# Performance work log

Hardware: AMD Instinct MI355X
Metric: run time of the kernel (lower is better)

Reference implementation:

```python
import jax, jax.numpy as jnp
import numpy as np

N_NODES = 50000


def binarize(w):
    # straight-through sign binarization (forward: sign, backward: identity)
    return w + jax.lax.stop_gradient(jnp.sign(w) - w)


def sage_conv(x, src, dst, w_l, b_l, w_r, num_nodes):
    # PyG SAGEConv with mean aggregation:
    # out[i] = lin_l(mean_{j in N(i)} x[j]) + lin_r(x[i])
    msgs = x[src]  # [E, F] gather from source nodes
    agg = jax.ops.segment_sum(msgs, dst, num_segments=num_nodes)  # [N, F]
    deg = jax.ops.segment_sum(jnp.ones_like(dst, dtype=x.dtype), dst,
                              num_segments=num_nodes)
    agg = agg / jnp.maximum(deg, 1.0)[:, None]
    return agg @ w_l.T + b_l + x @ w_r.T


def setup_inputs() -> dict:
    key = jax.random.key(0)
    ks = jax.random.split(key, 9)
    in_dim, hid, out_dim = 96, 128, 64
    x = jax.random.normal(ks[0], (N_NODES, in_dim), dtype=jnp.float32)
    edge_index = jax.random.randint(ks[1], (2, 800000), 0, N_NODES, dtype=jnp.int64)
    s1 = 1.0 / np.sqrt(in_dim)
    s2 = 1.0 / np.sqrt(hid)
    w1_l = jax.random.uniform(ks[2], (hid, in_dim), minval=-s1, maxval=s1)
    b1 = jax.random.uniform(ks[3], (hid,), minval=-s1, maxval=s1)
    w1_r = jax.random.uniform(ks[4], (hid, in_dim), minval=-s1, maxval=s1)
    w2_l = jax.random.uniform(ks[5], (out_dim, hid), minval=-s2, maxval=s2)
    b2 = jax.random.uniform(ks[6], (out_dim,), minval=-s2, maxval=s2)
    w2_r = jax.random.uniform(ks[7], (out_dim, hid), minval=-s2, maxval=s2)
    return {"x": x, "edge_index": edge_index, "w1_l": w1_l, "b1": b1,
            "w1_r": w1_r, "w2_l": w2_l, "b2": b2, "w2_r": w2_r}


def reference(x, edge_index, w1_l, b1, w1_r, w2_l, b2, w2_r):
    src, dst = edge_index[0], edge_index[1]
    h = sage_conv(x, src, dst, binarize(w1_l), b1, binarize(w1_r), N_NODES)
    h = jax.nn.relu(h)
    out = sage_conv(h, src, dst, binarize(w2_l), b2, binarize(w2_r), N_NODES)
    return jnp.squeeze(out, axis=-1) if out.shape[-1] == 1 else out
```

## Files before the change

### kernel.cpp

```cpp
#include <hip/hip_runtime.h>
#include <cstdint>
#include <cstddef>


#define N_NODES 50000
#define IN_DIM 96
#define HID 128
#define OUT_DIM 64
#define DCAP 64

typedef __attribute__((ext_vector_type(8))) short bf16x8;
typedef __attribute__((ext_vector_type(4))) float f32x4;

static inline size_t alignUp(size_t v, size_t a) { return (v + a - 1) & ~(a - 1); }

__device__ __forceinline__ uint16_t f2bf(float f) {
  uint32_t u = __float_as_uint(f);
  return (uint16_t)((u + 0x7FFF + ((u >> 16) & 1)) >> 16);
}
__device__ __forceinline__ float bflo(uint32_t v) { return __uint_as_float(v << 16); }
__device__ __forceinline__ float bfhi(uint32_t v) { return __uint_as_float(v & 0xFFFF0000u); }

__device__ __forceinline__ uint16_t sgnbf(float w) {
  return (w > 0.f) ? (uint16_t)0x3F80 : ((w < 0.f) ? (uint16_t)0xBF80 : (uint16_t)0);
}

#define NS1 (128 * 192)
#define NS2 (128 * 128)
#define NSCAT 1024

__global__ __launch_bounds__(256) void build_prep_kernel(
    const int* __restrict__ src, const int* __restrict__ dst,
    int* __restrict__ cnt, uint16_t* __restrict__ adj16, int E,
    const float* __restrict__ x,
    const float* __restrict__ w1l, const float* __restrict__ w1r,
    const float* __restrict__ w2l, const float* __restrict__ w2r,
    uint16_t* __restrict__ S1t, uint16_t* __restrict__ S2t,
    uint16_t* __restrict__ xb, int total4) {
  const int t = threadIdx.x;
  if ((int)blockIdx.x < NSCAT) {
    const int stride = NSCAT * 256;
    for (int i = blockIdx.x * 256 + t; i < E; i += stride) {
      const int d = dst[i];
      const int s = src[i];
      const int k = atomicAdd(&cnt[d], 1);
      if (k < DCAP) adj16[(d << 6) + k] = (uint16_t)s;
    }
  } else {
    const int idx = ((int)blockIdx.x - NSCAT) * 256 + t;
    if (idx < NS1) {
      int n = idx / 192, k = idx - n * 192;
      float w = (k < 96) ? w1l[n * 96 + k] : w1r[n * 96 + (k - 96)];
      S1t[idx] = sgnbf(w);
    } else if (idx < NS1 + NS2) {
      int i2 = idx - NS1;
      int n = i2 >> 7, k = i2 & 127;
      float w = (n < 64) ? w2l[n * 128 + k] : w2r[(n - 64) * 128 + k];
      S2t[i2] = sgnbf(w);
    } else {
      int i = idx - NS1 - NS2;
      if (i < total4) {
        float4 v = *(const float4*)(x + (size_t)i * 4);
        uint32_t p0 = (uint32_t)f2bf(v.x) | ((uint32_t)f2bf(v.y) << 16);
        uint32_t p1 = (uint32_t)f2bf(v.z) | ((uint32_t)f2bf(v.w) << 16);
        *(uint2*)(xb + (size_t)i * 4) = make_uint2(p0, p1);
      }
    }
  }
}

__global__ __launch_bounds__(256) void agg1_kernel(const uint16_t* __restrict__ xb,
    const uint16_t* __restrict__ adj16, const int* __restrict__ cnt,
    uint16_t* __restrict__ AGGb, int nNodes) {
  const int sg = threadIdx.x >> 4;
  const int j = threadIdx.x & 15;
  const int n = blockIdx.x * 16 + sg;
  if (n >= nNodes) return;
  const int deg = min(cnt[n], DCAP);
  const int beg = n << 6;
  const int end = beg + deg;
  const bool act = j < 12;
  const int foff = j * 8;
  float a0 = 0.f, a1 = 0.f, a2 = 0.f, a3 = 0.f, a4 = 0.f, a5 = 0.f, a6 = 0.f, a7 = 0.f;

  int e = beg;
  for (; e + 8 <= end; e += 8) {
    const uint4 av = *(const uint4*)(adj16 + e);
    const uint32_t s0 = av.x & 0xFFFFu, s1 = av.x >> 16;
    const uint32_t s2 = av.y & 0xFFFFu, s3 = av.y >> 16;
    const uint32_t s4 = av.z & 0xFFFFu, s5 = av.z >> 16;
    const uint32_t s6 = av.w & 0xFFFFu, s7 = av.w >> 16;
    uint4 v0 = make_uint4(0u,0u,0u,0u), v1 = v0, v2 = v0, v3 = v0;
    uint4 v4 = v0, v5 = v0, v6 = v0, v7 = v0;
    if (act) {
      v0 = *(const uint4*)(xb + (size_t)s0 * IN_DIM + foff);
      v1 = *(const uint4*)(xb + (size_t)s1 * IN_DIM + foff);
      v2 = *(const uint4*)(xb + (size_t)s2 * IN_DIM + foff);
      v3 = *(const uint4*)(xb + (size_t)s3 * IN_DIM + foff);
      v4 = *(const uint4*)(xb + (size_t)s4 * IN_DIM + foff);
      v5 = *(const uint4*)(xb + (size_t)s5 * IN_DIM + foff);
      v6 = *(const uint4*)(xb + (size_t)s6 * IN_DIM + foff);
      v7 = *(const uint4*)(xb + (size_t)s7 * IN_DIM + foff);
    }
    __builtin_amdgcn_sched_barrier(0);
    a0 += (bflo(v0.x) + bflo(v1.x) + bflo(v2.x) + bflo(v3.x)) + (bflo(v4.x) + bflo(v5.x) + bflo(v6.x) + bflo(v7.x));
    a1 += (bfhi(v0.x) + bfhi(v1.x) + bfhi(v2.x) + bfhi(v3.x)) + (bfhi(v4.x) + bfhi(v5.x) + bfhi(v6.x) + bfhi(v7.x));
    a2 += (bflo(v0.y) + bflo(v1.y) + bflo(v2.y) + bflo(v3.y)) + (bflo(v4.y) + bflo(v5.y) + bflo(v6.y) + bflo(v7.y));
    a3 += (bfhi(v0.y) + bfhi(v1.y) + bfhi(v2.y) + bfhi(v3.y)) + (bfhi(v4.y) + bfhi(v5.y) + bfhi(v6.y) + bfhi(v7.y));
    a4 += (bflo(v0.z) + bflo(v1.z) + bflo(v2.z) + bflo(v3.z)) + (bflo(v4.z) + bflo(v5.z) + bflo(v6.z) + bflo(v7.z));
    a5 += (bfhi(v0.z) + bfhi(v1.z) + bfhi(v2.z) + bfhi(v3.z)) + (bfhi(v4.z) + bfhi(v5.z) + bfhi(v6.z) + bfhi(v7.z));
    a6 += (bflo(v0.w) + bflo(v1.w) + bflo(v2.w) + bflo(v3.w)) + (bflo(v4.w) + bflo(v5.w) + bflo(v6.w) + bflo(v7.w));
    a7 += (bfhi(v0.w) + bfhi(v1.w) + bfhi(v2.w) + bfhi(v3.w)) + (bfhi(v4.w) + bfhi(v5.w) + bfhi(v6.w) + bfhi(v7.w));
  }
  if (e + 4 <= end) {
    const uint2 av = *(const uint2*)(adj16 + e);
    const uint32_t s0 = av.x & 0xFFFFu, s1 = av.x >> 16;
    const uint32_t s2 = av.y & 0xFFFFu, s3 = av.y >> 16;
    uint4 v0 = make_uint4(0u,0u,0u,0u), v1 = v0, v2 = v0, v3 = v0;
    if (act) {
      v0 = *(const uint4*)(xb + (size_t)s0 * IN_DIM + foff);
      v1 = *(const uint4*)(xb + (size_t)s1 * IN_DIM + foff);
      v2 = *(const uint4*)(xb + (size_t)s2 * IN_DIM + foff);
      v3 = *(const uint4*)(xb + (size_t)s3 * IN_DIM + foff);
    }
    __builtin_amdgcn_sched_barrier(0);
    a0 += bflo(v0.x) + bflo(v1.x) + bflo(v2.x) + bflo(v3.x);
    a1 += bfhi(v0.x) + bfhi(v1.x) + bfhi(v2.x) + bfhi(v3.x);
    a2 += bflo(v0.y) + bflo(v1.y) + bflo(v2.y) + bflo(v3.y);
    a3 += bfhi(v0.y) + bfhi(v1.y) + bfhi(v2.y) + bfhi(v3.y);
    a4 += bflo(v0.z) + bflo(v1.z) + bflo(v2.z) + bflo(v3.z);
    a5 += bfhi(v0.z) + bfhi(v1.z) + bfhi(v2.z) + bfhi(v3.z);
    a6 += bflo(v0.w) + bflo(v1.w) + bflo(v2.w) + bflo(v3.w);
    a7 += bfhi(v0.w) + bfhi(v1.w) + bfhi(v2.w) + bfhi(v3.w);
    e += 4;
  }
  for (; e < end; ++e) {
    const uint32_t s = adj16[e];
    uint4 v = make_uint4(0u,0u,0u,0u);
    if (act) v = *(const uint4*)(xb + (size_t)s * IN_DIM + foff);
    a0 += bflo(v.x); a1 += bfhi(v.x);
    a2 += bflo(v.y); a3 += bfhi(v.y);
    a4 += bflo(v.z); a5 += bfhi(v.z);
    a6 += bflo(v.w); a7 += bfhi(v.w);
  }
  if (act) {
    const float inv = 1.0f / (float)(deg > 1 ? deg : 1);
    uint4 o;
    o.x = (uint32_t)f2bf(a0 * inv) | ((uint32_t)f2bf(a1 * inv) << 16);
    o.y = (uint32_t)f2bf(a2 * inv) | ((uint32_t)f2bf(a3 * inv) << 16);
    o.z = (uint32_t)f2bf(a4 * inv) | ((uint32_t)f2bf(a5 * inv) << 16);
    o.w = (uint32_t)f2bf(a6 * inv) | ((uint32_t)f2bf(a7 * inv) << 16);
    *(uint4*)(AGGb + (size_t)n * IN_DIM + foff) = o;
  }
}

__global__ __launch_bounds__(256) void final_kernel(const uint16_t* __restrict__ T2b,
    const float* __restrict__ R2, const uint16_t* __restrict__ adj16,
    const int* __restrict__ cnt, float* __restrict__ out, int nNodes) {
  const int sg = threadIdx.x >> 4;
  const int j = threadIdx.x & 15;
  const int n = blockIdx.x * 16 + sg;
  if (n >= nNodes) return;
  const int deg = min(cnt[n], DCAP);
  const int beg = n << 6;
  const int end = beg + deg;
  const int foff = j * 4;
  float a0 = 0.f, a1 = 0.f, a2 = 0.f, a3 = 0.f;

  int e = beg;
  for (; e + 8 <= end; e += 8) {
    const uint4 av = *(const uint4*)(adj16 + e);
    const uint32_t s0 = av.x & 0xFFFFu, s1 = av.x >> 16;
    const uint32_t s2 = av.y & 0xFFFFu, s3 = av.y >> 16;
    const uint32_t s4 = av.z & 0xFFFFu, s5 = av.z >> 16;
    const uint32_t s6 = av.w & 0xFFFFu, s7 = av.w >> 16;
    const uint2 v0 = *(const uint2*)(T2b + (size_t)s0 * 64 + foff);
    const uint2 v1 = *(const uint2*)(T2b + (size_t)s1 * 64 + foff);
    const uint2 v2 = *(const uint2*)(T2b + (size_t)s2 * 64 + foff);
    const uint2 v3 = *(const uint2*)(T2b + (size_t)s3 * 64 + foff);
    const uint2 v4 = *(const uint2*)(T2b + (size_t)s4 * 64 + foff);
    const uint2 v5 = *(const uint2*)(T2b + (size_t)s5 * 64 + foff);
    const uint2 v6 = *(const uint2*)(T2b + (size_t)s6 * 64 + foff);
    const uint2 v7 = *(const uint2*)(T2b + (size_t)s7 * 64 + foff);
    __builtin_amdgcn_sched_barrier(0);
    a0 += (bflo(v0.x) + bflo(v1.x) + bflo(v2.x) + bflo(v3.x)) + (bflo(v4.x) + bflo(v5.x) + bflo(v6.x) + bflo(v7.x));
    a1 += (bfhi(v0.x) + bfhi(v1.x) + bfhi(v2.x) + bfhi(v3.x)) + (bfhi(v4.x) + bfhi(v5.x) + bfhi(v6.x) + bfhi(v7.x));
    a2 += (bflo(v0.y) + bflo(v1.y) + bflo(v2.y) + bflo(v3.y)) + (bflo(v4.y) + bflo(v5.y) + bflo(v6.y) + bflo(v7.y));
    a3 += (bfhi(v0.y) + bfhi(v1.y) + bfhi(v2.y) + bfhi(v3.y)) + (bfhi(v4.y) + bfhi(v5.y) + bfhi(v6.y) + bfhi(v7.y));
  }
  if (e + 4 <= end) {
    const uint2 av = *(const uint2*)(adj16 + e);
    const uint32_t s0 = av.x & 0xFFFFu, s1 = av.x >> 16;
    const uint32_t s2 = av.y & 0xFFFFu, s3 = av.y >> 16;
    const uint2 v0 = *(const uint2*)(T2b + (size_t)s0 * 64 + foff);
    const uint2 v1 = *(const uint2*)(T2b + (size_t)s1 * 64 + foff);
    const uint2 v2 = *(const uint2*)(T2b + (size_t)s2 * 64 + foff);
    const uint2 v3 = *(const uint2*)(T2b + (size_t)s3 * 64 + foff);
    __builtin_amdgcn_sched_barrier(0);
    a0 += bflo(v0.x) + bflo(v1.x) + bflo(v2.x) + bflo(v3.x);
    a1 += bfhi(v0.x) + bfhi(v1.x) + bfhi(v2.x) + bfhi(v3.x);
    a2 += bflo(v0.y) + bflo(v1.y) + bflo(v2.y) + bflo(v3.y);
    a3 += bfhi(v0.y) + bfhi(v1.y) + bfhi(v2.y) + bfhi(v3.y);
    e += 4;
  }
  for (; e < end; ++e) {
    const uint32_t s = adj16[e];
    const uint2 v = *(const uint2*)(T2b + (size_t)s * 64 + foff);
    a0 += bflo(v.x); a1 += bfhi(v.x);
    a2 += bflo(v.y); a3 += bfhi(v.y);
  }
  const float inv = 1.0f / (float)(deg > 1 ? deg : 1);
  const float4 r = *(const float4*)(R2 + (size_t)n * 64 + foff);
  float4 o;
  o.x = a0 * inv + r.x;
  o.y = a1 * inv + r.y;
  o.z = a2 * inv + r.z;
  o.w = a3 * inv + r.w;
  *(float4*)(out + (size_t)n * 64 + foff) = o;
}

#define SP1 200
#define SP2 136
#define HP 136
__global__ __launch_bounds__(256) void gemm12_kernel(
    const uint16_t* __restrict__ AGGb, const uint16_t* __restrict__ xb,
    const uint16_t* __restrict__ S1t, const uint16_t* __restrict__ S2t,
    const float* __restrict__ b1, const float* __restrict__ b2,
    uint16_t* __restrict__ T2b, float* __restrict__ R2, int M) {
  __shared__ uint16_t BS[128 * SP1];
  __shared__ uint16_t Hs[64 * HP];
  const int tid = threadIdx.x;
  const int wv = tid >> 6;
  const int lane = tid & 63;
  const int m16 = lane & 15;
  const int quad = lane >> 4;
  const int rowBase = blockIdx.x * 64 + wv * 16;
  int arow = rowBase + m16;
  if (arow >= M) arow = M - 1;
  const int kq = quad * 8;

#pragma unroll
  for (int i = 0; i < 12; ++i) {
    const int idx8 = tid + i * 256;
    const int col = idx8 / 24;
    const int k8 = (idx8 - col * 24) * 8;
    const bf16x8 v = *(const bf16x8*)(S1t + (size_t)idx8 * 8);
    *(bf16x8*)&BS[col * SP1 + k8] = v;
  }
  bf16x8 a1f[6];
#pragma unroll
  for (int s = 0; s < 3; ++s)
    a1f[s] = *(const bf16x8*)(AGGb + (size_t)arow * IN_DIM + s * 32 + kq);
#pragma unroll
  for (int s = 0; s < 3; ++s)
    a1f[3 + s] = *(const bf16x8*)(xb + (size_t)arow * IN_DIM + s * 32 + kq);
  __syncthreads();

  f32x4 acc1[8];
#pragma unroll
  for (int cf = 0; cf < 8; ++cf) acc1[cf] = (f32x4){0.f, 0.f, 0.f, 0.f};
#pragma unroll
  for (int s = 0; s < 6; ++s) {
#pragma unroll
    for (int cf = 0; cf < 8; ++cf) {
      const bf16x8 b = *(const bf16x8*)&BS[(cf * 16 + m16) * SP1 + s * 32 + kq];
      acc1[cf] = __builtin_amdgcn_mfma_f32_16x16x32_bf16(a1f[s], b, acc1[cf], 0, 0, 0);
    }
  }

#pragma unroll
  for (int cf = 0; cf < 8; ++cf) {
    const int col = cf * 16 + m16;
    const float bias = b1[col];
#pragma unroll
    for (int r = 0; r < 4; ++r) {
      const float v = fmaxf(acc1[cf][r] + bias, 0.f);
      Hs[(wv * 16 + quad * 4 + r) * HP + col] = f2bf(v);
    }
  }
  __syncthreads();

#pragma unroll
  for (int i = 0; i < 8; ++i) {
    const int idx8 = tid + i * 256;
    const int col = idx8 >> 4;
    const int k8 = (idx8 & 15) * 8;
    const bf16x8 v = *(const bf16x8*)(S2t + (size_t)idx8 * 8);
    *(bf16x8*)&BS[col * SP2 + k8] = v;
  }
  __syncthreads();

  f32x4 acc2[8];
#pragma unroll
  for (int cf = 0; cf < 8; ++cf) acc2[cf] = (f32x4){0.f, 0.f, 0.f, 0.f};
#pragma unroll
  for (int s = 0; s < 4; ++s) {
    const bf16x8 a = *(const bf16x8*)&Hs[(wv * 16 + m16) * HP + s * 32 + kq];
#pragma unroll
    for (int cf = 0; cf < 8; ++cf) {
      const bf16x8 b = *(const bf16x8*)&BS[(cf * 16 + m16) * SP2 + s * 32 + kq];
      acc2[cf] = __builtin_amdgcn_mfma_f32_16x16x32_bf16(a, b, acc2[cf], 0, 0, 0);
    }
  }

#pragma unroll
  for (int cf = 0; cf < 8; ++cf) {
    const int col = cf * 16 + m16;
#pragma unroll
    for (int r = 0; r < 4; ++r) {
      const int row = rowBase + quad * 4 + r;
      if (row < M) {
        const float v = acc2[cf][r];
        if (col < 64) {
          T2b[(size_t)row * 64 + col] = f2bf(v);
        } else {
          R2[(size_t)row * 64 + (col - 64)] = v + b2[col - 64];
        }
      }
    }
  }
}

extern "C" void kernel_launch(void* const* d_in, const int* in_sizes, int n_in,
                              void* d_out, int out_size, void* d_ws, size_t ws_size,
                              hipStream_t stream) {
  const float* x   = (const float*)d_in[0];
  const int*   ei  = (const int*)d_in[1];
  const float* w1l = (const float*)d_in[2];
  const float* b1  = (const float*)d_in[3];
  const float* w1r = (const float*)d_in[4];
  const float* w2l = (const float*)d_in[5];
  const float* b2  = (const float*)d_in[6];
  const float* w2r = (const float*)d_in[7];
  float* out = (float*)d_out;

  const int N = in_sizes[0] / IN_DIM;
  const int E = in_sizes[1] / 2;
  const int* src = ei;
  const int* dst = ei + E;

  char* p = (char*)d_ws;
  uint16_t* AGGb = (uint16_t*)p; p += alignUp((size_t)N * IN_DIM * sizeof(uint16_t), 256);
  uint16_t* T2b  = (uint16_t*)p; p += alignUp((size_t)N * 64 * sizeof(uint16_t), 256);
  float* R2      = (float*)p;    p += alignUp((size_t)N * 64 * sizeof(float), 256);
  uint16_t* xb = (uint16_t*)p; p += alignUp((size_t)N * IN_DIM * sizeof(uint16_t), 256);
  uint16_t* S1t = (uint16_t*)p; p += alignUp(NS1 * sizeof(uint16_t), 256);
  uint16_t* S2t = (uint16_t*)p; p += alignUp(NS2 * sizeof(uint16_t), 256);
  uint16_t* adj16 = (uint16_t*)p; p += alignUp((size_t)N * DCAP * sizeof(uint16_t), 256);
  int* cnt = (int*)p; p += alignUp((size_t)N * sizeof(int), 256);
  (void)ws_size; (void)n_in; (void)out_size;

  hipMemsetAsync(cnt, 0, (size_t)N * sizeof(int), stream);

  const int total4 = N * IN_DIM / 4;
  const int prepThreads = NS1 + NS2 + total4;
  const int nPrep = (prepThreads + 255) / 256;
  build_prep_kernel<<<NSCAT + nPrep, 256, 0, stream>>>(
      src, dst, cnt, adj16, E,
      x, w1l, w1r, w2l, w2r, S1t, S2t, xb, total4);

  const int nodeBlocks16 = (N + 15) / 16;
  agg1_kernel<<<nodeBlocks16, 256, 0, stream>>>(xb, adj16, cnt, AGGb, N);

  const int gemmBlocks = (N + 63) / 64;
  gemm12_kernel<<<gemmBlocks, 256, 0, stream>>>(AGGb, xb, S1t, S2t, b1, b2, T2b, R2, N);

  final_kernel<<<nodeBlocks16, 256, 0, stream>>>(T2b, R2, adj16, cnt, out, N);
}
```

Measured before the change: 190.8 us.

## Build adjacency via two-pass bucketed scatter with shared-memory atomics

Replaces the per-edge global atomicAdd on node counters with a two-pass approach. First, edges are binned into 256-node buckets using shared-memory histograms and one global atomic per bucket per chunk. Then a per-bucket kernel builds node counts and adjacency lists with shared-memory atomics. This targets global atomic contention and scattered writes, at the cost of an extra kernel, a large staging buffer, and a fixed bucket capacity (CAP) that could overflow and drop edges.

```diff
diff --git a/kernel.cpp b/kernel.cpp
--- a/kernel.cpp
+++ b/kernel.cpp
@@ -8,6 +8,7 @@
 #define HID 128
 #define OUT_DIM 64
 #define DCAP 64
+#define CAP 6144
 
 typedef __attribute__((ext_vector_type(8))) short bf16x8;
 typedef __attribute__((ext_vector_type(4))) float f32x4;
@@ -27,27 +28,40 @@
 
 #define NS1 (128 * 192)
 #define NS2 (128 * 128)
-#define NSCAT 1024
-
-__global__ __launch_bounds__(256) void build_prep_kernel(
+#define SCAT_CHUNK 2048
+
+__global__ __launch_bounds__(256) void scatter_prep_kernel(
     const int* __restrict__ src, const int* __restrict__ dst,
-    int* __restrict__ cnt, uint16_t* __restrict__ adj16, int E,
+    int* __restrict__ bucketCursor, uint32_t* __restrict__ bucketBuf,
+    int E, int nScat,
     const float* __restrict__ x,
     const float* __restrict__ w1l, const float* __restrict__ w1r,
     const float* __restrict__ w2l, const float* __restrict__ w2r,
     uint16_t* __restrict__ S1t, uint16_t* __restrict__ S2t,
     uint16_t* __restrict__ xb, int total4) {
+  __shared__ int h[256];
+  __shared__ int g[256];
+  __shared__ int c[256];
   const int t = threadIdx.x;
-  if ((int)blockIdx.x < NSCAT) {
-    const int stride = NSCAT * 256;
-    for (int i = blockIdx.x * 256 + t; i < E; i += stride) {
+  if ((int)blockIdx.x < nScat) {
+    const int base = blockIdx.x * SCAT_CHUNK;
+    const int end = min(base + SCAT_CHUNK, E);
+    h[t] = 0;
+    __syncthreads();
+    for (int i = base + t; i < end; i += 256)
+      atomicAdd(&h[dst[i] >> 8], 1);
+    __syncthreads();
+    if (h[t]) g[t] = t * CAP + atomicAdd(&bucketCursor[t], h[t]);
+    c[t] = 0;
+    __syncthreads();
+    for (int i = base + t; i < end; i += 256) {
       const int d = dst[i];
-      const int s = src[i];
-      const int k = atomicAdd(&cnt[d], 1);
-      if (k < DCAP) adj16[(d << 6) + k] = (uint16_t)s;
+      const int b = d >> 8;
+      const int ticket = atomicAdd(&c[b], 1);
+      bucketBuf[g[b] + ticket] = (uint32_t)src[i] | ((uint32_t)(d & 255) << 16);
     }
   } else {
-    const int idx = ((int)blockIdx.x - NSCAT) * 256 + t;
+    const int idx = ((int)blockIdx.x - nScat) * 256 + t;
     if (idx < NS1) {
       int n = idx / 192, k = idx - n * 192;
       float w = (k < 96) ? w1l[n * 96 + k] : w1r[n * 96 + (k - 96)];
@@ -66,6 +80,33 @@
         *(uint2*)(xb + (size_t)i * 4) = make_uint2(p0, p1);
       }
     }
+  }
+}
+
+__global__ __launch_bounds__(256) void bucket_build_kernel(const uint32_t* __restrict__ bucketBuf,
+    const int* __restrict__ bucketCursor, int* __restrict__ cnt,
+    uint16_t* __restrict__ adj16, int N) {
+  __shared__ int h[256];
+  __shared__ int cur[256];
+  const int t = threadIdx.x;
+  const int b = blockIdx.x;
+  const int nodeBase = b << 8;
+  const int beg = b * CAP;
+  const int m = min(bucketCursor[b], CAP);
+  h[t] = 0;
+  cur[t] = 0;
+  __syncthreads();
+  for (int i = t; i < m; i += 256)
+    atomicAdd(&h[(bucketBuf[beg + i] >> 16) & 255], 1);
+  __syncthreads();
+  const int node = nodeBase + t;
+  if (node < N) cnt[node] = h[t];
+  for (int i = t; i < m; i += 256) {
+    const uint32_t u = bucketBuf[beg + i];
+    const int ld = (u >> 16) & 255;
+    const int ticket = atomicAdd(&cur[ld], 1);
+    if (ticket < DCAP)
+      adj16[((nodeBase + ld) << 6) + ticket] = (uint16_t)(u & 0xFFFFu);
   }
 }
 
@@ -338,6 +379,7 @@
   const int E = in_sizes[1] / 2;
   const int* src = ei;
   const int* dst = ei + E;
+  const int NB = (N + 255) >> 8;
 
   char* p = (char*)d_ws;
   uint16_t* AGGb = (uint16_t*)p; p += alignUp((size_t)N * IN_DIM * sizeof(uint16_t), 256);
@@ -348,16 +390,21 @@
   uint16_t* S2t = (uint16_t*)p; p += alignUp(NS2 * sizeof(uint16_t), 256);
   uint16_t* adj16 = (uint16_t*)p; p += alignUp((size_t)N * DCAP * sizeof(uint16_t), 256);
   int* cnt = (int*)p; p += alignUp((size_t)N * sizeof(int), 256);
+  uint32_t* bucketBuf = (uint32_t*)p; p += alignUp((size_t)NB * CAP * sizeof(uint32_t), 256);
+  int* bucketCursor = (int*)p; p += alignUp(256 * sizeof(int), 256);
   (void)ws_size; (void)n_in; (void)out_size;
 
-  hipMemsetAsync(cnt, 0, (size_t)N * sizeof(int), stream);
-
+  hipMemsetAsync(bucketCursor, 0, 256 * sizeof(int), stream);
+
+  const int nScat = (E + SCAT_CHUNK - 1) / SCAT_CHUNK;
   const int total4 = N * IN_DIM / 4;
   const int prepThreads = NS1 + NS2 + total4;
   const int nPrep = (prepThreads + 255) / 256;
-  build_prep_kernel<<<NSCAT + nPrep, 256, 0, stream>>>(
-      src, dst, cnt, adj16, E,
+  scatter_prep_kernel<<<nScat + nPrep, 256, 0, stream>>>(
+      src, dst, bucketCursor, bucketBuf, E, nScat,
       x, w1l, w1r, w2l, w2r, S1t, S2t, xb, total4);
+
+  bucket_build_kernel<<<NB, 256, 0, stream>>>(bucketBuf, bucketCursor, cnt, adj16, N);
 
   const int nodeBlocks16 = (N + 15) / 16;
   agg1_kernel<<<nodeBlocks16, 256, 0, stream>>>(xb, adj16, cnt, AGGb, N);
```

Result: faster. 173.2 us (-9.2%).
